# Performance work log

Measured on AMD Instinct MI355X. Metric: run time of the kernel, lower is better.

## Reference

```python
import jax, jax.numpy as jnp
import numpy as np

NUM_HEADS = 4
NUM_GROUPS = 8
EPS = 1e-5


def group_norm(x, w, b):
    # x: [N, C, H, W], normalize over (C//G, H, W) per group
    N, C, H, W = x.shape
    xg = x.reshape(N, NUM_GROUPS, C // NUM_GROUPS, H, W)
    mu = jnp.mean(xg, axis=(2, 3, 4), keepdims=True)
    var = jnp.var(xg, axis=(2, 3, 4), keepdims=True)
    xn = ((xg - mu) * jax.lax.rsqrt(var + EPS)).reshape(N, C, H, W)
    return xn * w[None, :, None, None] + b[None, :, None, None]


def conv1x1(x, w, b):
    # x: [N, C, H, W], w: [Cout, Cin], b: [Cout]
    return jnp.einsum('nchw,dc->ndhw', x, w) + b[None, :, None, None]


def setup_inputs() -> dict:
    key = jax.random.key(0)
    ks = jax.random.split(key, 12)
    N, C, H, W = 2, 256, 64, 64
    s = 1.0 / np.sqrt(C)
    inp = {
        'x': jax.random.normal(ks[0], (N, C, H, W), jnp.float32),
        'mask': jax.random.randint(ks[1], (N, 1, H, W), 0, 2, jnp.int32),
        'norm_w': jnp.ones((C,), jnp.float32),
        'norm_b': jnp.zeros((C,), jnp.float32),
        'q_w': jax.random.normal(ks[2], (C, C), jnp.float32) * s,
        'q_b': jnp.zeros((C,), jnp.float32),
        'k_w': jax.random.normal(ks[3], (C, C), jnp.float32) * s,
        'k_b': jnp.zeros((C,), jnp.float32),
        'v_w': jax.random.normal(ks[4], (C, C), jnp.float32) * s,
        'v_b': jnp.zeros((C,), jnp.float32),
        'p_w': jax.random.normal(ks[5], (C, C), jnp.float32) * s,
        'p_b': jnp.zeros((C,), jnp.float32),
    }
    return inp


def reference(x, mask, norm_w, norm_b, q_w, q_b, k_w, k_b, v_w, v_b, p_w, p_b):
    N, C, H, W = x.shape
    hd = C // NUM_HEADS  # head dim
    L = H * W
    xn = group_norm(x, norm_w, norm_b)
    q = conv1x1(xn, q_w, q_b).reshape(N, NUM_HEADS, hd, L)
    k = conv1x1(xn, k_w, k_b).reshape(N, NUM_HEADS, hd, L)
    v = conv1x1(xn, v_w, v_b).reshape(N, NUM_HEADS, hd, L)
    scores = jnp.einsum('nhcl,nhck->nhlk', q, k) * (hd ** -0.5)
    probs = jax.nn.softmax(scores, axis=-1)
    out = jnp.einsum('nhlk,nhck->nhcl', probs, v).reshape(N, C, H, W)
    out = conv1x1(out, p_w, p_b)
    return (x + out, mask)
```

## Files before the change

kernel.cpp:

```cpp
#include <hip/hip_runtime.h>
#include <hip/hip_bf16.h>

#define NBATCH 2
#define CCH    256
#define LLEN   4096
#define NGROUP 8
#define CPG    32
#define NHEAD  4
#define HD     64
#define GEPS   1e-5f
#define QSCALE 0.18033688011112042f


typedef short bf16x8 __attribute__((ext_vector_type(8)));
typedef float f32x4  __attribute__((ext_vector_type(4)));

__device__ __forceinline__ unsigned short f2b(float f) {
  unsigned u = __float_as_uint(f);
  u += 0x7FFFu + ((u >> 16) & 1u);
  return (unsigned short)(u >> 16);
}
__device__ __forceinline__ unsigned cvtpk(float lo, float hi) {
  unsigned r;
  asm("v_cvt_pk_bf16_f32 %0, %1, %2" : "=v"(r) : "v"(lo), "v"(hi));
  return r;
}
__device__ __forceinline__ float exp2_(float x) {
#if __has_builtin(__builtin_amdgcn_exp2f)
  return __builtin_amdgcn_exp2f(x);
#else
  return exp2f(x);
#endif
}

__global__ __launch_bounds__(256) void setup_kernel(const float* __restrict__ x,
                                                    float* __restrict__ part) {
  __shared__ float rs[4], rss[4];
  const int sb = blockIdx.x;
  const int t = threadIdx.x;
  const int gidx = sb >> 4, sub = sb & 15;
  const float4* xp = (const float4*)(x + (size_t)gidx * (CPG * LLEN)) + (size_t)sub * 2048;
  float s = 0.f, ss = 0.f;
  for (int i = t; i < 2048; i += 256) {
    const float4 v = xp[i];
    s += v.x + v.y + v.z + v.w;
    ss = fmaf(v.x, v.x, ss);
    ss = fmaf(v.y, v.y, ss);
    ss = fmaf(v.z, v.z, ss);
    ss = fmaf(v.w, v.w, ss);
  }
#pragma unroll
  for (int off = 32; off; off >>= 1) {
    s  += __shfl_down(s, off);
    ss += __shfl_down(ss, off);
  }
  if ((t & 63) == 0) { rs[t >> 6] = s; rss[t >> 6] = ss; }
  __syncthreads();
  if (t == 0) {
    part[sb * 2 + 0] = rs[0] + rs[1] + rs[2] + rs[3];
    part[sb * 2 + 1] = rss[0] + rss[1] + rss[2] + rss[3];
  }
}

__global__ __launch_bounds__(256) void gn_apply_kernel(
    const float* __restrict__ x, const float* __restrict__ w,
    const float* __restrict__ b, const float* __restrict__ part,
    const float* __restrict__ qw, const float* __restrict__ kw,
    const float* __restrict__ vw, const float* __restrict__ pw,
    const float* __restrict__ qb, const float* __restrict__ kb,
    const float* __restrict__ vb, const float* __restrict__ pb,
    const int* __restrict__ mask,
    unsigned short* __restrict__ xn16, unsigned short* __restrict__ w16,
    float* __restrict__ bias_ws, float* __restrict__ out2) {
  __shared__ float tile[32][68];
  const int bx = blockIdx.x;
  const int t = threadIdx.x;
  if (bx < 1024) {
    const int lx = bx & 63, cy = (bx >> 6) & 7, n = bx >> 9;
    const int l0 = lx * 64, c0 = cy * 32;
    const int g16 = n * 8 + cy;
    float s = 0.f, ss = 0.f;
#pragma unroll
    for (int i = 0; i < 16; i++) {
      s  += part[(g16 * 16 + i) * 2 + 0];
      ss += part[(g16 * 16 + i) * 2 + 1];
    }
    const float inv_cnt = 1.0f / (float)(CPG * LLEN);
    const float mu = s * inv_cnt;
    const float rsg = rsqrtf(ss * inv_cnt - mu * mu + GEPS);
    const int cl = t >> 3, l8 = t & 7;
    const float aa = rsg * w[c0 + cl];
    const float dd = b[c0 + cl] - mu * aa;
    const float* xrow = x + ((size_t)n * CCH + c0 + cl) * LLEN + l0;
#pragma unroll
    for (int i = 0; i < 2; i++) {
      const int ll = (l8 + 8 * i) * 4;
      float4 v = *(const float4*)(xrow + ll);
      v.x = fmaf(v.x, aa, dd);
      v.y = fmaf(v.y, aa, dd);
      v.z = fmaf(v.z, aa, dd);
      v.w = fmaf(v.w, aa, dd);
      *(float4*)&tile[cl][ll] = v;
    }
    __syncthreads();
    const int l = t & 63, cg = t >> 6;
    const int labs = l0 + l;
    bf16x8 ov;
#pragma unroll
    for (int j = 0; j < 8; j++) ov[j] = (short)f2b(tile[cg * 8 + j][l]);
    const size_t pos = (((size_t)n * 256 + (labs >> 4)) * 8 + (c0 >> 5)) * 512 +
                       ((labs & 15) + 16 * cg) * 8;
    *(bf16x8*)(xn16 + pos) = ov;
  } else if (bx < 1280) {
    const int sb = bx - 1024;
    const int idx = sb * 256 + t;
    const int m = idx >> 14;
    const int rem = idx & 16383;
    const int cout = rem >> 6;
    const int ch4 = (rem & 63) << 2;
    const float* srcp = (m == 0) ? qw : (m == 1) ? kw : (m == 2) ? vw : pw;
    const float sc = (m == 0) ? QSCALE : 1.0f;
    const float4 v = ((const float4*)srcp)[(size_t)cout * 64 + (ch4 >> 2)];
    unsigned short* dst = w16 +
        ((size_t)(m * 16 + (cout >> 4)) * 8 + (ch4 >> 5)) * 512 +
        ((cout & 15) + 16 * ((ch4 >> 3) & 3)) * 8 + (ch4 & 7);
    uint2 wd;
    wd.x = cvtpk(v.x * sc, v.y * sc);
    wd.y = cvtpk(v.z * sc, v.w * sc);
    *(uint2*)dst = wd;
    if (sb == 0) {
      bias_ws[t]       = qb[t] * QSCALE;
      bias_ws[256 + t] = kb[t];
      bias_ws[512 + t] = vb[t];
      bias_ws[768 + t] = pb[t];
    }
  } else {
    const int i = (bx - 1280) * 256 + t;
    out2[i] = (float)mask[i];
  }
}

__global__ __launch_bounds__(256, 4) void qkv_mfma_kernel(
    const unsigned short* __restrict__ xn16,
    const unsigned short* __restrict__ w16,
    const float* __restrict__ bias_ws,
    unsigned short* __restrict__ q16,
    unsigned short* __restrict__ k16,
    unsigned short* __restrict__ v16) {
  const int t = threadIdx.x;
  const int lane = t & 63, wv = t >> 6;
  const int col = lane & 15, quad = lane >> 4;
  const int m0 = blockIdx.x * 32;
  const int wsel = blockIdx.y;
  const int n = m0 >> 12;
  const int m16b = (m0 & 4095) >> 4;
  const int l0 = m0 & 4095;

  const unsigned short* xnb = xn16 + (((size_t)n * 256 + m16b) * 8) * 512 + lane * 8;
  const unsigned short* wb  = w16 + ((size_t)(wsel * 16 + wv * 4) * 8) * 512 + lane * 8;

  f32x4 acc[2][4];
#pragma unroll
  for (int mt = 0; mt < 2; mt++)
#pragma unroll
    for (int ct = 0; ct < 4; ct++) acc[mt][ct] = {0.f, 0.f, 0.f, 0.f};

#pragma unroll
  for (int kc = 0; kc < 8; kc++) {
    bf16x8 xf[2], wf[4];
    xf[0] = *(const bf16x8*)(xnb + (size_t)kc * 512);
    xf[1] = *(const bf16x8*)(xnb + (size_t)(8 + kc) * 512);
#pragma unroll
    for (int ct = 0; ct < 4; ct++)
      wf[ct] = *(const bf16x8*)(wb + (size_t)(ct * 8 + kc) * 512);
#pragma unroll
    for (int mt = 0; mt < 2; mt++)
#pragma unroll
      for (int ct = 0; ct < 4; ct++)
        acc[mt][ct] = (wsel < 2)
            ? __builtin_amdgcn_mfma_f32_16x16x32_bf16(wf[ct], xf[mt], acc[mt][ct], 0, 0, 0)
            : __builtin_amdgcn_mfma_f32_16x16x32_bf16(xf[mt], wf[ct], acc[mt][ct], 0, 0, 0);
  }

  if (wsel < 2) {
    unsigned short* dst = (wsel == 0) ? q16 : k16;
#pragma unroll
    for (int ct = 0; ct < 4; ct++) {
      const float4 b4 = *(const float4*)&bias_ws[wsel * CCH + wv * 64 + ct * 16 + quad * 4];
#pragma unroll
      for (int mt = 0; mt < 2; mt++) {
        uint2 wd;
        wd.x = cvtpk(acc[mt][ct][0] + b4.x, acc[mt][ct][1] + b4.y);
        wd.y = cvtpk(acc[mt][ct][2] + b4.z, acc[mt][ct][3] + b4.w);
        *(uint2*)(dst + ((size_t)(n * 256 + m16b + mt) * 8 + wv * 2 + (ct >> 1)) * 512 +
                  (col + 16 * ((ct & 1) * 2 + (quad >> 1))) * 8 + (quad & 1) * 4) = wd;
      }
    }
  } else {
#pragma unroll
    for (int ct = 0; ct < 4; ct++) {
      const float bv = bias_ws[2 * CCH + wv * 64 + ct * 16 + col];
#pragma unroll
      for (int mt = 0; mt < 2; mt++) {
        uint2 wd;
        wd.x = cvtpk(acc[mt][ct][0] + bv, acc[mt][ct][1] + bv);
        wd.y = cvtpk(acc[mt][ct][2] + bv, acc[mt][ct][3] + bv);
        *(uint2*)(v16 + (((size_t)n * 128 + (l0 >> 5)) * 16 + wv * 4 + ct) * 512 +
                  (col + 16 * (mt * 2 + (quad >> 1))) * 8 + (quad & 1) * 4) = wd;
      }
    }
  }
}

__global__ __launch_bounds__(256, 2) void attn_mfma_kernel(
    const unsigned short* __restrict__ q16,
    const unsigned short* __restrict__ k16,
    const unsigned short* __restrict__ v16,
    unsigned short* __restrict__ o16) {
  __shared__ __align__(16) unsigned char shraw[20480];
  f32x4 (*red)[4][64] = (f32x4 (*)[4][64])shraw;
  f32x4 (*lred)[64] = (f32x4 (*)[64])(shraw + 16384);
  const int t = threadIdx.x;
  const int lane = t & 63, wv = t >> 6;
  const int col = lane & 15, quad = lane >> 4;
  const int fid = blockIdx.y * gridDim.x + blockIdx.x;
  const int nh = fid & 7, qx = fid >> 3;
  const int n = nh >> 2, h = nh & 3;
  const int hc = h * HD;
  const int qt0 = qx * 4;

  const unsigned short* qb = q16 + (size_t)n * (256 * 8 * 512);
  const unsigned short* kb = k16 + (size_t)n * (256 * 8 * 512);
  const unsigned short* vb = v16 + (size_t)n * (128 * 16 * 512);

  bf16x8 bq[4][2];
#pragma unroll
  for (int qt = 0; qt < 4; qt++)
#pragma unroll
    for (int ks = 0; ks < 2; ks++)
      bq[qt][ks] = *(const bf16x8*)(qb + ((size_t)(qt0 + qt) * 8 + h * 2 + ks) * 512 + lane * 8);

  bf16x8 bones;
#pragma unroll
  for (int i = 0; i < 8; i++) bones[i] = (short)0x3F80;
  const f32x4 zf = {0.f, 0.f, 0.f, 0.f};

  f32x4 o[4][4], lacc[4];
#pragma unroll
  for (int qt = 0; qt < 4; qt++) {
    lacc[qt] = {0.f, 0.f, 0.f, 0.f};
#pragma unroll
    for (int ct = 0; ct < 4; ct++) o[qt][ct] = {0.f, 0.f, 0.f, 0.f};
  }

  const unsigned short* kp = kb + ((size_t)(wv * 64) * 8 + h * 2) * 512 + lane * 8;
  const unsigned short* vp = vb + ((size_t)(wv * 32) * 16 + h * 4) * 512 + lane * 8;

  bf16x8 kA[2][2], kB[2][2], vA[4], vB[4];
  auto loadK = [&](bf16x8 (&kr)[2][2], const unsigned short* p) {
#pragma unroll
    for (int kt = 0; kt < 2; kt++)
#pragma unroll
      for (int ks = 0; ks < 2; ks++)
        kr[kt][ks] = *(const bf16x8*)(p + kt * 4096 + ks * 512);
  };
  auto loadV = [&](bf16x8 (&vv)[4], const unsigned short* p) {
#pragma unroll
    for (int ct = 0; ct < 4; ct++) vv[ct] = *(const bf16x8*)(p + ct * 512);
  };

  auto chunk = [&](bf16x8 (&kr)[2][2], bf16x8 (&vv)[4]) {
    bf16x8 pa[4];
#pragma unroll
    for (int qt = 0; qt < 4; qt++) {
      unsigned a0, a1, b0, b1;
      {
        f32x4 s = __builtin_amdgcn_mfma_f32_16x16x32_bf16(kr[0][0], bq[qt][0], zf, 0, 0, 0);
        s = __builtin_amdgcn_mfma_f32_16x16x32_bf16(kr[0][1], bq[qt][1], s, 0, 0, 0);
        a0 = cvtpk(exp2_(s[0]), exp2_(s[1]));
        a1 = cvtpk(exp2_(s[2]), exp2_(s[3]));
      }
      {
        f32x4 s = __builtin_amdgcn_mfma_f32_16x16x32_bf16(kr[1][0], bq[qt][0], zf, 0, 0, 0);
        s = __builtin_amdgcn_mfma_f32_16x16x32_bf16(kr[1][1], bq[qt][1], s, 0, 0, 0);
        b0 = cvtpk(exp2_(s[0]), exp2_(s[1]));
        b1 = cvtpk(exp2_(s[2]), exp2_(s[3]));
      }
      auto r0 = __builtin_amdgcn_permlane32_swap(a0, b0, false, false);
      auto s0 = __builtin_amdgcn_permlane16_swap(r0[0], r0[1], false, false);
      auto r1 = __builtin_amdgcn_permlane32_swap(a1, b1, false, false);
      auto s1 = __builtin_amdgcn_permlane16_swap(r1[0], r1[1], false, false);
      union { unsigned u[4]; bf16x8 v; } pu;
      pu.u[0] = s0[0];
      pu.u[1] = s1[0];
      pu.u[2] = s0[1];
      pu.u[3] = s1[1];
      pa[qt] = pu.v;
    }
    __builtin_amdgcn_s_setprio(1);
#pragma unroll
    for (int qt = 0; qt < 4; qt++) {
      lacc[qt] = __builtin_amdgcn_mfma_f32_16x16x32_bf16(pa[qt], bones, lacc[qt], 0, 0, 0);
#pragma unroll
      for (int ct = 0; ct < 4; ct++)
        o[qt][ct] = __builtin_amdgcn_mfma_f32_16x16x32_bf16(pa[qt], vv[ct], o[qt][ct], 0, 0, 0);
    }
    __builtin_amdgcn_s_setprio(0);
  };

  loadK(kA, kp);
  loadV(vA, vp);
  for (int it = 0; it < 30; it += 2) {
    loadK(kB, kp + 8192);
    loadV(vB, vp + 8192);
    chunk(kA, vA);
    kp += 16384;
    vp += 16384;
    loadK(kA, kp);
    loadV(vA, vp);
    chunk(kB, vB);
  }
  loadK(kB, kp + 8192);
  loadV(vB, vp + 8192);
  chunk(kA, vA);
  chunk(kB, vB);

  const int cch = hc + wv * 16 + col;
  const int lquad16 = 16 * ((cch >> 3) & 3);
  const size_t ctile = cch >> 5;
#pragma unroll
  for (int qt = 0; qt < 4; qt++) {
    __syncthreads();
#pragma unroll
    for (int ct = 0; ct < 4; ct++) red[wv][ct][lane] = o[qt][ct];
    lred[wv][lane] = lacc[qt];
    __syncthreads();
    f32x4 os = red[0][wv][lane];
    os += red[1][wv][lane];
    os += red[2][wv][lane];
    os += red[3][wv][lane];
    f32x4 ls = lred[0][lane];
    ls += lred[1][lane];
    ls += lred[2][lane];
    ls += lred[3][lane];
    const size_t base = (((size_t)n * 256 + qt0 + qt) * 8 + ctile) * 512 + (cch & 7);
#pragma unroll
    for (int r = 0; r < 4; r++)
      o16[base + ((quad * 4 + r) + lquad16) * 8] = f2b(os[r] / ls[r]);
  }
}

__global__ __launch_bounds__(256, 4) void proj_mfma_kernel(
    const unsigned short* __restrict__ o16,
    const unsigned short* __restrict__ w16,
    const float* __restrict__ pbias,
    const float* __restrict__ x,
    float* __restrict__ out) {
  const int t = threadIdx.x;
  const int lane = t & 63, wv = t >> 6;
  const int col = lane & 15, quad = lane >> 4;
  const int m0 = blockIdx.x * 32;
  const int by = blockIdx.y;
  const int co0 = by * 64;
  const int n = m0 >> 12, l0 = m0 & 4095;

  const unsigned short* ob = o16 + (size_t)n * (256 * 8 * 512);
  const unsigned short* wb = w16 + ((size_t)(48 + by * 4 + wv) * 8) * 512 + lane * 8;

  f32x4 acc[2];
#pragma unroll
  for (int i = 0; i < 2; i++) acc[i] = {0.f, 0.f, 0.f, 0.f};

#pragma unroll
  for (int kc = 0; kc < 8; kc++) {
    const bf16x8 aw = *(const bf16x8*)(wb + (size_t)kc * 512);
#pragma unroll
    for (int lt = 0; lt < 2; lt++) {
      const bf16x8 bo = *(const bf16x8*)(ob + ((size_t)((l0 >> 4) + lt) * 8 + kc) * 512 + lane * 8);
      acc[lt] = __builtin_amdgcn_mfma_f32_16x16x32_bf16(aw, bo, acc[lt], 0, 0, 0);
    }
  }
#pragma unroll
  for (int lt = 0; lt < 2; lt++)
#pragma unroll
    for (int r = 0; r < 4; r++) {
      const int cout = co0 + wv * 16 + quad * 4 + r;
      const size_t idx = ((size_t)(n * CCH + cout)) * LLEN + l0 + lt * 16 + col;
      out[idx] = acc[lt][r] + pbias[cout] + x[idx];
    }
}

extern "C" void kernel_launch(void* const* d_in, const int* in_sizes, int n_in,
                              void* d_out, int out_size, void* d_ws, size_t ws_size,
                              hipStream_t stream) {
  (void)in_sizes; (void)n_in; (void)out_size; (void)ws_size;
  const float* x      = (const float*)d_in[0];
  const int*   mask   = (const int*)d_in[1];
  const float* norm_w = (const float*)d_in[2];
  const float* norm_b = (const float*)d_in[3];
  const float* q_w    = (const float*)d_in[4];
  const float* q_b    = (const float*)d_in[5];
  const float* k_w    = (const float*)d_in[6];
  const float* k_b    = (const float*)d_in[7];
  const float* v_w    = (const float*)d_in[8];
  const float* v_b    = (const float*)d_in[9];
  const float* p_w    = (const float*)d_in[10];
  const float* p_b    = (const float*)d_in[11];

  const size_t TSZ = (size_t)NBATCH * LLEN * CCH;
  unsigned short* xn16 = (unsigned short*)d_ws;
  unsigned short* q16  = xn16 + TSZ;
  unsigned short* k16  = q16 + TSZ;
  unsigned short* v16  = k16 + TSZ;
  unsigned short* o16  = v16 + TSZ;
  unsigned short* w16  = o16 + TSZ;
  float* bias_ws = (float*)(w16 + 4 * 65536);
  float* part    = bias_ws + 1024;

  float* out  = (float*)d_out;
  float* out2 = out + TSZ;

  setup_kernel<<<256, 256, 0, stream>>>(x, part);
  gn_apply_kernel<<<1312, 256, 0, stream>>>(
      x, norm_w, norm_b, part, q_w, k_w, v_w, p_w, q_b, k_b, v_b, p_b,
      mask, xn16, w16, bias_ws, out2);
  qkv_mfma_kernel<<<dim3((NBATCH * LLEN) / 32, 3), 256, 0, stream>>>(
      xn16, w16, bias_ws, q16, k16, v16);
  attn_mfma_kernel<<<dim3(LLEN / 64, NBATCH * NHEAD), 256, 0, stream>>>(
      q16, k16, v16, o16);
  proj_mfma_kernel<<<dim3((NBATCH * LLEN) / 32, CCH / 64), 256, 0, stream>>>(
      o16, w16, bias_ws + 768, x, out);
}
```

Measured before the change: 142.5 us.

## Fuse group-norm stats into apply kernel via atomics; software-pipeline attention loop

Merges the separate group-norm statistics kernel into the apply kernel. Each block accumulates partial sums with atomics, then spins on a per-group counter until all 64 blocks of its group have contributed. This saves one launch and a second read of x, but relies on every block being co-resident, since the spin-wait can deadlock otherwise. The attention inner loop is also split into QK-exp, permute and PV stages, software-pipelined across two buffers so exp and permlane work overlaps the PV MFMAs.

```diff
diff --git a/kernel.cpp b/kernel.cpp
--- a/kernel.cpp
+++ b/kernel.cpp
@@ -33,87 +33,51 @@
 #endif
 }
 
-__global__ __launch_bounds__(256) void setup_kernel(const float* __restrict__ x,
-                                                    float* __restrict__ part) {
-  __shared__ float rs[4], rss[4];
-  const int sb = blockIdx.x;
-  const int t = threadIdx.x;
-  const int gidx = sb >> 4, sub = sb & 15;
-  const float4* xp = (const float4*)(x + (size_t)gidx * (CPG * LLEN)) + (size_t)sub * 2048;
-  float s = 0.f, ss = 0.f;
-  for (int i = t; i < 2048; i += 256) {
-    const float4 v = xp[i];
-    s += v.x + v.y + v.z + v.w;
-    ss = fmaf(v.x, v.x, ss);
-    ss = fmaf(v.y, v.y, ss);
-    ss = fmaf(v.z, v.z, ss);
-    ss = fmaf(v.w, v.w, ss);
-  }
-#pragma unroll
-  for (int off = 32; off; off >>= 1) {
-    s  += __shfl_down(s, off);
-    ss += __shfl_down(ss, off);
-  }
-  if ((t & 63) == 0) { rs[t >> 6] = s; rss[t >> 6] = ss; }
-  __syncthreads();
-  if (t == 0) {
-    part[sb * 2 + 0] = rs[0] + rs[1] + rs[2] + rs[3];
-    part[sb * 2 + 1] = rss[0] + rss[1] + rss[2] + rss[3];
-  }
-}
-
-__global__ __launch_bounds__(256) void gn_apply_kernel(
-    const float* __restrict__ x, const float* __restrict__ w,
-    const float* __restrict__ b, const float* __restrict__ part,
+__global__ __launch_bounds__(256, 8) void gn_fused_kernel(
+    const float* __restrict__ x, const float* __restrict__ gw,
+    const float* __restrict__ gb,
     const float* __restrict__ qw, const float* __restrict__ kw,
     const float* __restrict__ vw, const float* __restrict__ pw,
     const float* __restrict__ qb, const float* __restrict__ kb,
     const float* __restrict__ vb, const float* __restrict__ pb,
     const int* __restrict__ mask,
     unsigned short* __restrict__ xn16, unsigned short* __restrict__ w16,
-    float* __restrict__ bias_ws, float* __restrict__ out2) {
+    float* __restrict__ bias_ws, float* __restrict__ gstat,
+    unsigned* __restrict__ gcnt, float* __restrict__ out2) {
   __shared__ float tile[32][68];
-  const int bx = blockIdx.x;
-  const int t = threadIdx.x;
-  if (bx < 1024) {
-    const int lx = bx & 63, cy = (bx >> 6) & 7, n = bx >> 9;
-    const int l0 = lx * 64, c0 = cy * 32;
-    const int g16 = n * 8 + cy;
-    float s = 0.f, ss = 0.f;
-#pragma unroll
-    for (int i = 0; i < 16; i++) {
-      s  += part[(g16 * 16 + i) * 2 + 0];
-      ss += part[(g16 * 16 + i) * 2 + 1];
-    }
-    const float inv_cnt = 1.0f / (float)(CPG * LLEN);
-    const float mu = s * inv_cnt;
-    const float rsg = rsqrtf(ss * inv_cnt - mu * mu + GEPS);
-    const int cl = t >> 3, l8 = t & 7;
-    const float aa = rsg * w[c0 + cl];
-    const float dd = b[c0 + cl] - mu * aa;
-    const float* xrow = x + ((size_t)n * CCH + c0 + cl) * LLEN + l0;
-#pragma unroll
-    for (int i = 0; i < 2; i++) {
-      const int ll = (l8 + 8 * i) * 4;
-      float4 v = *(const float4*)(xrow + ll);
-      v.x = fmaf(v.x, aa, dd);
-      v.y = fmaf(v.y, aa, dd);
-      v.z = fmaf(v.z, aa, dd);
-      v.w = fmaf(v.w, aa, dd);
-      *(float4*)&tile[cl][ll] = v;
-    }
-    __syncthreads();
-    const int l = t & 63, cg = t >> 6;
-    const int labs = l0 + l;
-    bf16x8 ov;
-#pragma unroll
-    for (int j = 0; j < 8; j++) ov[j] = (short)f2b(tile[cg * 8 + j][l]);
-    const size_t pos = (((size_t)n * 256 + (labs >> 4)) * 8 + (c0 >> 5)) * 512 +
-                       ((labs & 15) + 16 * cg) * 8;
-    *(bf16x8*)(xn16 + pos) = ov;
-  } else if (bx < 1280) {
-    const int sb = bx - 1024;
-    const int idx = sb * 256 + t;
+  __shared__ float sred[8];
+  __shared__ float smu, srsg;
+  const int bx = blockIdx.x, t = threadIdx.x;
+  const int lx = bx & 63, cy = (bx >> 6) & 7, n = bx >> 9;
+  const int l0 = lx * 64, c0 = cy * 32;
+  const int g = n * 8 + cy;
+  const int cl = t >> 3, l8 = t & 7;
+  const float* xrow = x + ((size_t)n * CCH + c0 + cl) * LLEN + l0;
+  const float4 va = ((const float4*)xrow)[l8];
+  const float4 vb2 = ((const float4*)xrow)[l8 + 8];
+  float s = va.x + va.y + va.z + va.w + vb2.x + vb2.y + vb2.z + vb2.w;
+  float ss = 0.f;
+  ss = fmaf(va.x, va.x, ss);  ss = fmaf(va.y, va.y, ss);
+  ss = fmaf(va.z, va.z, ss);  ss = fmaf(va.w, va.w, ss);
+  ss = fmaf(vb2.x, vb2.x, ss); ss = fmaf(vb2.y, vb2.y, ss);
+  ss = fmaf(vb2.z, vb2.z, ss); ss = fmaf(vb2.w, vb2.w, ss);
+#pragma unroll
+  for (int off = 32; off; off >>= 1) {
+    s  += __shfl_down(s, off);
+    ss += __shfl_down(ss, off);
+  }
+  if ((t & 63) == 0) { sred[t >> 6] = s; sred[4 + (t >> 6)] = ss; }
+  __syncthreads();
+  if (t == 0) {
+    const float S = sred[0] + sred[1] + sred[2] + sred[3];
+    const float SS = sred[4] + sred[5] + sred[6] + sred[7];
+    atomicAdd(&gstat[g], S);
+    atomicAdd(&gstat[16 + g], SS);
+    __threadfence();
+    __hip_atomic_fetch_add(&gcnt[g], 1u, __ATOMIC_RELEASE, __HIP_MEMORY_SCOPE_AGENT);
+  }
+  if (t < 64) {
+    const int idx = bx * 64 + t;
     const int m = idx >> 14;
     const int rem = idx & 16383;
     const int cout = rem >> 6;
@@ -128,16 +92,50 @@
     wd.x = cvtpk(v.x * sc, v.y * sc);
     wd.y = cvtpk(v.z * sc, v.w * sc);
     *(uint2*)dst = wd;
-    if (sb == 0) {
-      bias_ws[t]       = qb[t] * QSCALE;
-      bias_ws[256 + t] = kb[t];
-      bias_ws[512 + t] = vb[t];
-      bias_ws[768 + t] = pb[t];
-    }
-  } else {
-    const int i = (bx - 1280) * 256 + t;
+  } else if (t < 72) {
+    const int i = bx * 8 + (t - 64);
     out2[i] = (float)mask[i];
-  }
+  } else if (t == 72) {
+    const int m = bx >> 8, c = bx & 255;
+    bias_ws[bx] = (m == 0) ? qb[c] * QSCALE : (m == 1) ? kb[c]
+                : (m == 2) ? vb[c] : pb[c];
+  }
+  const float wc = gw[c0 + cl], bc = gb[c0 + cl];
+  if (t == 0) {
+    while (__hip_atomic_load(&gcnt[g], __ATOMIC_ACQUIRE,
+                             __HIP_MEMORY_SCOPE_AGENT) < 64u)
+      __builtin_amdgcn_s_sleep(2);
+    const float S = __hip_atomic_load(&gstat[g], __ATOMIC_RELAXED,
+                                      __HIP_MEMORY_SCOPE_AGENT);
+    const float SS = __hip_atomic_load(&gstat[16 + g], __ATOMIC_RELAXED,
+                                       __HIP_MEMORY_SCOPE_AGENT);
+    const float inv = 1.0f / (float)(CPG * LLEN);
+    const float mu = S * inv;
+    smu = mu;
+    srsg = rsqrtf(SS * inv - mu * mu + GEPS);
+  }
+  __syncthreads();
+  const float aa = srsg * wc;
+  const float dd = bc - smu * aa;
+  {
+    float4 u = va, v = vb2;
+    u.x = fmaf(u.x, aa, dd); u.y = fmaf(u.y, aa, dd);
+    u.z = fmaf(u.z, aa, dd); u.w = fmaf(u.w, aa, dd);
+    v.x = fmaf(v.x, aa, dd); v.y = fmaf(v.y, aa, dd);
+    v.z = fmaf(v.z, aa, dd); v.w = fmaf(v.w, aa, dd);
+    *(float4*)&tile[cl][l8 * 4] = u;
+    *(float4*)&tile[cl][(l8 + 8) * 4] = v;
+  }
+  __syncthreads();
+  const int l = t & 63, cg = t >> 6;
+  const int labs = l0 + l;
+  union { unsigned u[4]; bf16x8 v; } ov;
+#pragma unroll
+  for (int j = 0; j < 4; j++)
+    ov.u[j] = cvtpk(tile[cg * 8 + 2 * j][l], tile[cg * 8 + 2 * j + 1][l]);
+  const size_t pos = (((size_t)n * 256 + (labs >> 4)) * 8 + (c0 >> 5)) * 512 +
+                     ((labs & 15) + 16 * cg) * 8;
+  *(bf16x8*)(xn16 + pos) = ov.v;
 }
 
 __global__ __launch_bounds__(256, 4) void qkv_mfma_kernel(
@@ -257,6 +255,9 @@
   const unsigned short* vp = vb + ((size_t)(wv * 32) * 16 + h * 4) * 512 + lane * 8;
 
   bf16x8 kA[2][2], kB[2][2], vA[4], vB[4];
+  unsigned pkA[4][4], pkB[4][4];
+  bf16x8 paA[4], paB[4];
+
   auto loadK = [&](bf16x8 (&kr)[2][2], const unsigned short* p) {
 #pragma unroll
     for (int kt = 0; kt < 2; kt++)
@@ -268,27 +269,25 @@
 #pragma unroll
     for (int ct = 0; ct < 4; ct++) vv[ct] = *(const bf16x8*)(p + ct * 512);
   };
-
-  auto chunk = [&](bf16x8 (&kr)[2][2], bf16x8 (&vv)[4]) {
-    bf16x8 pa[4];
+  auto QKE = [&](unsigned (&pk)[4][4], bf16x8 (&kr)[2][2]) {
 #pragma unroll
     for (int qt = 0; qt < 4; qt++) {
-      unsigned a0, a1, b0, b1;
-      {
-        f32x4 s = __builtin_amdgcn_mfma_f32_16x16x32_bf16(kr[0][0], bq[qt][0], zf, 0, 0, 0);
-        s = __builtin_amdgcn_mfma_f32_16x16x32_bf16(kr[0][1], bq[qt][1], s, 0, 0, 0);
-        a0 = cvtpk(exp2_(s[0]), exp2_(s[1]));
-        a1 = cvtpk(exp2_(s[2]), exp2_(s[3]));
-      }
-      {
-        f32x4 s = __builtin_amdgcn_mfma_f32_16x16x32_bf16(kr[1][0], bq[qt][0], zf, 0, 0, 0);
-        s = __builtin_amdgcn_mfma_f32_16x16x32_bf16(kr[1][1], bq[qt][1], s, 0, 0, 0);
-        b0 = cvtpk(exp2_(s[0]), exp2_(s[1]));
-        b1 = cvtpk(exp2_(s[2]), exp2_(s[3]));
-      }
-      auto r0 = __builtin_amdgcn_permlane32_swap(a0, b0, false, false);
+      f32x4 sa = __builtin_amdgcn_mfma_f32_16x16x32_bf16(kr[0][0], bq[qt][0], zf, 0, 0, 0);
+      sa = __builtin_amdgcn_mfma_f32_16x16x32_bf16(kr[0][1], bq[qt][1], sa, 0, 0, 0);
+      f32x4 sb = __builtin_amdgcn_mfma_f32_16x16x32_bf16(kr[1][0], bq[qt][0], zf, 0, 0, 0);
+      sb = __builtin_amdgcn_mfma_f32_16x16x32_bf16(kr[1][1], bq[qt][1], sb, 0, 0, 0);
+      pk[qt][0] = cvtpk(exp2_(sa[0]), exp2_(sa[1]));
+      pk[qt][1] = cvtpk(exp2_(sa[2]), exp2_(sa[3]));
+      pk[qt][2] = cvtpk(exp2_(sb[0]), exp2_(sb[1]));
+      pk[qt][3] = cvtpk(exp2_(sb[2]), exp2_(sb[3]));
+    }
+  };
+  auto PERM = [&](bf16x8 (&pa)[4], unsigned (&pk)[4][4]) {
+#pragma unroll
+    for (int qt = 0; qt < 4; qt++) {
+      auto r0 = __builtin_amdgcn_permlane32_swap(pk[qt][0], pk[qt][2], false, false);
       auto s0 = __builtin_amdgcn_permlane16_swap(r0[0], r0[1], false, false);
-      auto r1 = __builtin_amdgcn_permlane32_swap(a1, b1, false, false);
+      auto r1 = __builtin_amdgcn_permlane32_swap(pk[qt][1], pk[qt][3], false, false);
       auto s1 = __builtin_amdgcn_permlane16_swap(r1[0], r1[1], false, false);
       union { unsigned u[4]; bf16x8 v; } pu;
       pu.u[0] = s0[0];
@@ -297,6 +296,8 @@
       pu.u[3] = s1[1];
       pa[qt] = pu.v;
     }
+  };
+  auto PV = [&](bf16x8 (&pa)[4], bf16x8 (&vv)[4]) {
     __builtin_amdgcn_s_setprio(1);
 #pragma unroll
     for (int qt = 0; qt < 4; qt++) {
@@ -308,22 +309,27 @@
     __builtin_amdgcn_s_setprio(0);
   };
 
-  loadK(kA, kp);
-  loadV(vA, vp);
+  loadK(kA, kp); loadV(vA, vp);
+  QKE(pkA, kA);
+  loadK(kB, kp + 8192); loadV(vB, vp + 8192);
   for (int it = 0; it < 30; it += 2) {
-    loadK(kB, kp + 8192);
-    loadV(vB, vp + 8192);
-    chunk(kA, vA);
-    kp += 16384;
-    vp += 16384;
-    loadK(kA, kp);
-    loadV(vA, vp);
-    chunk(kB, vB);
-  }
-  loadK(kB, kp + 8192);
-  loadV(vB, vp + 8192);
-  chunk(kA, vA);
-  chunk(kB, vB);
+    PERM(paA, pkA);
+    loadK(kA, kp + 16384);
+    QKE(pkB, kB);
+    PV(paA, vA);
+    loadK(kB, kp + 24576);
+    loadV(vA, vp + 16384);
+    PERM(paB, pkB);
+    QKE(pkA, kA);
+    PV(paB, vB);
+    loadV(vB, vp + 24576);
+    kp += 16384; vp += 16384;
+  }
+  PERM(paA, pkA);
+  QKE(pkB, kB);
+  PV(paA, vA);
+  PERM(paB, pkB);
+  PV(paB, vB);
 
   const int cch = hc + wv * 16 + col;
   const int lquad16 = 16 * ((cch >> 3) & 3);
@@ -415,15 +421,16 @@
   unsigned short* o16  = v16 + TSZ;
   unsigned short* w16  = o16 + TSZ;
   float* bias_ws = (float*)(w16 + 4 * 65536);
-  float* part    = bias_ws + 1024;
+  float* gstat   = bias_ws + 1024;
+  unsigned* gcnt = (unsigned*)(gstat + 32);
 
   float* out  = (float*)d_out;
   float* out2 = out + TSZ;
 
-  setup_kernel<<<256, 256, 0, stream>>>(x, part);
-  gn_apply_kernel<<<1312, 256, 0, stream>>>(
-      x, norm_w, norm_b, part, q_w, k_w, v_w, p_w, q_b, k_b, v_b, p_b,
-      mask, xn16, w16, bias_ws, out2);
+  hipMemsetAsync(gstat, 0, (32 + 16) * sizeof(float), stream);
+  gn_fused_kernel<<<1024, 256, 0, stream>>>(
+      x, norm_w, norm_b, q_w, k_w, v_w, p_w, q_b, k_b, v_b, p_b,
+      mask, xn16, w16, bias_ws, gstat, gcnt, out2);
   qkv_mfma_kernel<<<dim3((NBATCH * LLEN) / 32, 3), 256, 0, stream>>>(
       xn16, w16, bias_ws, q16, k16, v16);
   attn_mfma_kernel<<<dim3(LLEN / 64, NBATCH * NHEAD), 256, 0, stream>>>(
```

Result: slower. 192.6 us (+35.1%).

## Software-pipeline attention loop so QK^T/exp of next chunk overlaps PV of current

Applied to the files above, without the earlier changes.

Splits the per-chunk attention body into QK+exp, permute, and PV stages, then reorders the main loop so the score/exp computation for chunk i+1 is issued alongside the PV MFMAs of chunk i. The goal is to overlap the transcendental and VALU work with matrix-core work and to hide the dependency stall between the score MFMAs and their exp. It keeps more registers live (two packed-probability buffers and two permuted operand sets), which risks lower occupancy or spills.

```diff
diff --git a/kernel.cpp b/kernel.cpp
--- a/kernel.cpp
+++ b/kernel.cpp
@@ -257,6 +257,9 @@
   const unsigned short* vp = vb + ((size_t)(wv * 32) * 16 + h * 4) * 512 + lane * 8;
 
   bf16x8 kA[2][2], kB[2][2], vA[4], vB[4];
+  unsigned pkA[4][4], pkB[4][4];
+  bf16x8 paA[4], paB[4];
+
   auto loadK = [&](bf16x8 (&kr)[2][2], const unsigned short* p) {
 #pragma unroll
     for (int kt = 0; kt < 2; kt++)
@@ -268,27 +271,25 @@
 #pragma unroll
     for (int ct = 0; ct < 4; ct++) vv[ct] = *(const bf16x8*)(p + ct * 512);
   };
-
-  auto chunk = [&](bf16x8 (&kr)[2][2], bf16x8 (&vv)[4]) {
-    bf16x8 pa[4];
+  auto QKE = [&](unsigned (&pk)[4][4], bf16x8 (&kr)[2][2]) {
 #pragma unroll
     for (int qt = 0; qt < 4; qt++) {
-      unsigned a0, a1, b0, b1;
-      {
-        f32x4 s = __builtin_amdgcn_mfma_f32_16x16x32_bf16(kr[0][0], bq[qt][0], zf, 0, 0, 0);
-        s = __builtin_amdgcn_mfma_f32_16x16x32_bf16(kr[0][1], bq[qt][1], s, 0, 0, 0);
-        a0 = cvtpk(exp2_(s[0]), exp2_(s[1]));
-        a1 = cvtpk(exp2_(s[2]), exp2_(s[3]));
-      }
-      {
-        f32x4 s = __builtin_amdgcn_mfma_f32_16x16x32_bf16(kr[1][0], bq[qt][0], zf, 0, 0, 0);
-        s = __builtin_amdgcn_mfma_f32_16x16x32_bf16(kr[1][1], bq[qt][1], s, 0, 0, 0);
-        b0 = cvtpk(exp2_(s[0]), exp2_(s[1]));
-        b1 = cvtpk(exp2_(s[2]), exp2_(s[3]));
-      }
-      auto r0 = __builtin_amdgcn_permlane32_swap(a0, b0, false, false);
+      f32x4 sa = __builtin_amdgcn_mfma_f32_16x16x32_bf16(kr[0][0], bq[qt][0], zf, 0, 0, 0);
+      sa = __builtin_amdgcn_mfma_f32_16x16x32_bf16(kr[0][1], bq[qt][1], sa, 0, 0, 0);
+      f32x4 sb = __builtin_amdgcn_mfma_f32_16x16x32_bf16(kr[1][0], bq[qt][0], zf, 0, 0, 0);
+      sb = __builtin_amdgcn_mfma_f32_16x16x32_bf16(kr[1][1], bq[qt][1], sb, 0, 0, 0);
+      pk[qt][0] = cvtpk(exp2_(sa[0]), exp2_(sa[1]));
+      pk[qt][1] = cvtpk(exp2_(sa[2]), exp2_(sa[3]));
+      pk[qt][2] = cvtpk(exp2_(sb[0]), exp2_(sb[1]));
+      pk[qt][3] = cvtpk(exp2_(sb[2]), exp2_(sb[3]));
+    }
+  };
+  auto PERM = [&](bf16x8 (&pa)[4], unsigned (&pk)[4][4]) {
+#pragma unroll
+    for (int qt = 0; qt < 4; qt++) {
+      auto r0 = __builtin_amdgcn_permlane32_swap(pk[qt][0], pk[qt][2], false, false);
       auto s0 = __builtin_amdgcn_permlane16_swap(r0[0], r0[1], false, false);
-      auto r1 = __builtin_amdgcn_permlane32_swap(a1, b1, false, false);
+      auto r1 = __builtin_amdgcn_permlane32_swap(pk[qt][1], pk[qt][3], false, false);
       auto s1 = __builtin_amdgcn_permlane16_swap(r1[0], r1[1], false, false);
       union { unsigned u[4]; bf16x8 v; } pu;
       pu.u[0] = s0[0];
@@ -297,6 +298,8 @@
       pu.u[3] = s1[1];
       pa[qt] = pu.v;
     }
+  };
+  auto PV = [&](bf16x8 (&pa)[4], bf16x8 (&vv)[4]) {
     __builtin_amdgcn_s_setprio(1);
 #pragma unroll
     for (int qt = 0; qt < 4; qt++) {
@@ -308,22 +311,27 @@
     __builtin_amdgcn_s_setprio(0);
   };
 
-  loadK(kA, kp);
-  loadV(vA, vp);
+  loadK(kA, kp); loadV(vA, vp);
+  QKE(pkA, kA);
+  loadK(kB, kp + 8192); loadV(vB, vp + 8192);
   for (int it = 0; it < 30; it += 2) {
-    loadK(kB, kp + 8192);
-    loadV(vB, vp + 8192);
-    chunk(kA, vA);
-    kp += 16384;
-    vp += 16384;
-    loadK(kA, kp);
-    loadV(vA, vp);
-    chunk(kB, vB);
-  }
-  loadK(kB, kp + 8192);
-  loadV(vB, vp + 8192);
-  chunk(kA, vA);
-  chunk(kB, vB);
+    PERM(paA, pkA);
+    loadK(kA, kp + 16384);
+    QKE(pkB, kB);
+    PV(paA, vA);
+    loadK(kB, kp + 24576);
+    loadV(vA, vp + 16384);
+    PERM(paB, pkB);
+    QKE(pkA, kA);
+    PV(paB, vB);
+    loadV(vB, vp + 24576);
+    kp += 16384; vp += 16384;
+  }
+  PERM(paA, pkA);
+  QKE(pkB, kB);
+  PV(paA, vA);
+  PERM(paB, pkB);
+  PV(paB, vB);
 
   const int cch = hc + wv * 16 + col;
   const int lquad16 = 16 * ((cch >> 3) & 3);
```

New measurement: 143.7 us. No clear change (+0.8%).

## Fuse Q projection into attention kernel prologue, drop Q global buffer

Applied to the files above, without the earlier changes.

Q is no longer computed by the QKV kernel and written to global memory. Each attention block now computes its 64-query, single-head Q tile from the normalized input and Q weights with MFMA, rearranges it with permlane swaps into the expected fragment layout, and stages it through shared memory. This removes a third of the QKV grid plus the Q write and read traffic. In exchange, each attention block adds a short GEMM prologue and a barrier before its main loop.

```diff
diff --git a/kernel.cpp b/kernel.cpp
--- a/kernel.cpp
+++ b/kernel.cpp
@@ -144,14 +144,13 @@
     const unsigned short* __restrict__ xn16,
     const unsigned short* __restrict__ w16,
     const float* __restrict__ bias_ws,
-    unsigned short* __restrict__ q16,
     unsigned short* __restrict__ k16,
     unsigned short* __restrict__ v16) {
   const int t = threadIdx.x;
   const int lane = t & 63, wv = t >> 6;
   const int col = lane & 15, quad = lane >> 4;
   const int m0 = blockIdx.x * 32;
-  const int wsel = blockIdx.y;
+  const int wsel = blockIdx.y + 1;
   const int n = m0 >> 12;
   const int m16b = (m0 & 4095) >> 4;
   const int l0 = m0 & 4095;
@@ -177,13 +176,12 @@
     for (int mt = 0; mt < 2; mt++)
 #pragma unroll
       for (int ct = 0; ct < 4; ct++)
-        acc[mt][ct] = (wsel < 2)
+        acc[mt][ct] = (wsel == 1)
             ? __builtin_amdgcn_mfma_f32_16x16x32_bf16(wf[ct], xf[mt], acc[mt][ct], 0, 0, 0)
             : __builtin_amdgcn_mfma_f32_16x16x32_bf16(xf[mt], wf[ct], acc[mt][ct], 0, 0, 0);
   }
 
-  if (wsel < 2) {
-    unsigned short* dst = (wsel == 0) ? q16 : k16;
+  if (wsel == 1) {
 #pragma unroll
     for (int ct = 0; ct < 4; ct++) {
       const float4 b4 = *(const float4*)&bias_ws[wsel * CCH + wv * 64 + ct * 16 + quad * 4];
@@ -192,7 +190,7 @@
         uint2 wd;
         wd.x = cvtpk(acc[mt][ct][0] + b4.x, acc[mt][ct][1] + b4.y);
         wd.y = cvtpk(acc[mt][ct][2] + b4.z, acc[mt][ct][3] + b4.w);
-        *(uint2*)(dst + ((size_t)(n * 256 + m16b + mt) * 8 + wv * 2 + (ct >> 1)) * 512 +
+        *(uint2*)(k16 + ((size_t)(n * 256 + m16b + mt) * 8 + wv * 2 + (ct >> 1)) * 512 +
                   (col + 16 * ((ct & 1) * 2 + (quad >> 1))) * 8 + (quad & 1) * 4) = wd;
       }
     }
@@ -213,13 +211,16 @@
 }
 
 __global__ __launch_bounds__(256, 2) void attn_mfma_kernel(
-    const unsigned short* __restrict__ q16,
+    const unsigned short* __restrict__ xn16,
+    const unsigned short* __restrict__ w16,
+    const float* __restrict__ bias_ws,
     const unsigned short* __restrict__ k16,
     const unsigned short* __restrict__ v16,
     unsigned short* __restrict__ o16) {
   __shared__ __align__(16) unsigned char shraw[20480];
   f32x4 (*red)[4][64] = (f32x4 (*)[4][64])shraw;
   f32x4 (*lred)[64] = (f32x4 (*)[64])(shraw + 16384);
+  bf16x8 (*qlds)[2][64] = (bf16x8 (*)[2][64])shraw;
   const int t = threadIdx.x;
   const int lane = t & 63, wv = t >> 6;
   const int col = lane & 15, quad = lane >> 4;
@@ -229,21 +230,55 @@
   const int hc = h * HD;
   const int qt0 = qx * 4;
 
-  const unsigned short* qb = q16 + (size_t)n * (256 * 8 * 512);
+  const unsigned short* xb = xn16 + (size_t)n * (256 * 8 * 512);
   const unsigned short* kb = k16 + (size_t)n * (256 * 8 * 512);
   const unsigned short* vb = v16 + (size_t)n * (128 * 16 * 512);
 
-  bf16x8 bq[4][2];
-#pragma unroll
-  for (int qt = 0; qt < 4; qt++)
-#pragma unroll
-    for (int ks = 0; ks < 2; ks++)
-      bq[qt][ks] = *(const bf16x8*)(qb + ((size_t)(qt0 + qt) * 8 + h * 2 + ks) * 512 + lane * 8);
-
   bf16x8 bones;
 #pragma unroll
   for (int i = 0; i < 8; i++) bones[i] = (short)0x3F80;
   const f32x4 zf = {0.f, 0.f, 0.f, 0.f};
+
+  {
+    const unsigned short* xq = xb + ((size_t)(qt0 + wv) * 8) * 512 + lane * 8;
+    bf16x8 xf[8];
+#pragma unroll
+    for (int kc = 0; kc < 8; kc++) xf[kc] = *(const bf16x8*)(xq + (size_t)kc * 512);
+#pragma unroll
+    for (int ks = 0; ks < 2; ks++) {
+      const int g = h * 2 + ks;
+      f32x4 da = zf, db = zf;
+#pragma unroll
+      for (int kc = 0; kc < 8; kc++) {
+        const bf16x8 wf0 = *(const bf16x8*)(w16 + ((size_t)((2 * g + 0) * 8 + kc)) * 512 + lane * 8);
+        const bf16x8 wf1 = *(const bf16x8*)(w16 + ((size_t)((2 * g + 1) * 8 + kc)) * 512 + lane * 8);
+        da = __builtin_amdgcn_mfma_f32_16x16x32_bf16(wf0, xf[kc], da, 0, 0, 0);
+        db = __builtin_amdgcn_mfma_f32_16x16x32_bf16(wf1, xf[kc], db, 0, 0, 0);
+      }
+      const float4 ba = *(const float4*)&bias_ws[g * 32 + 0 * 16 + quad * 4];
+      const float4 bb = *(const float4*)&bias_ws[g * 32 + 1 * 16 + quad * 4];
+      const unsigned a0 = cvtpk(da[0] + ba.x, da[1] + ba.y);
+      const unsigned a1 = cvtpk(da[2] + ba.z, da[3] + ba.w);
+      const unsigned b0 = cvtpk(db[0] + bb.x, db[1] + bb.y);
+      const unsigned b1 = cvtpk(db[2] + bb.z, db[3] + bb.w);
+      auto r0 = __builtin_amdgcn_permlane32_swap(a0, b0, false, false);
+      auto s0 = __builtin_amdgcn_permlane16_swap(r0[0], r0[1], false, false);
+      auto r1 = __builtin_amdgcn_permlane32_swap(a1, b1, false, false);
+      auto s1 = __builtin_amdgcn_permlane16_swap(r1[0], r1[1], false, false);
+      union { unsigned u[4]; bf16x8 v; } pu;
+      pu.u[0] = s0[0];
+      pu.u[1] = s1[0];
+      pu.u[2] = s0[1];
+      pu.u[3] = s1[1];
+      qlds[wv][ks][lane] = pu.v;
+    }
+  }
+  __syncthreads();
+  bf16x8 bq[4][2];
+#pragma unroll
+  for (int qt = 0; qt < 4; qt++)
+#pragma unroll
+    for (int ks = 0; ks < 2; ks++) bq[qt][ks] = qlds[qt][ks][lane];
 
   f32x4 o[4][4], lacc[4];
 #pragma unroll
@@ -409,8 +444,7 @@
 
   const size_t TSZ = (size_t)NBATCH * LLEN * CCH;
   unsigned short* xn16 = (unsigned short*)d_ws;
-  unsigned short* q16  = xn16 + TSZ;
-  unsigned short* k16  = q16 + TSZ;
+  unsigned short* k16  = xn16 + TSZ;
   unsigned short* v16  = k16 + TSZ;
   unsigned short* o16  = v16 + TSZ;
   unsigned short* w16  = o16 + TSZ;
@@ -424,10 +458,10 @@
   gn_apply_kernel<<<1312, 256, 0, stream>>>(
       x, norm_w, norm_b, part, q_w, k_w, v_w, p_w, q_b, k_b, v_b, p_b,
       mask, xn16, w16, bias_ws, out2);
-  qkv_mfma_kernel<<<dim3((NBATCH * LLEN) / 32, 3), 256, 0, stream>>>(
-      xn16, w16, bias_ws, q16, k16, v16);
+  qkv_mfma_kernel<<<dim3((NBATCH * LLEN) / 32, 2), 256, 0, stream>>>(
+      xn16, w16, bias_ws, k16, v16);
   attn_mfma_kernel<<<dim3(LLEN / 64, NBATCH * NHEAD), 256, 0, stream>>>(
-      q16, k16, v16, o16);
+      xn16, w16, bias_ws, k16, v16, o16);
   proj_mfma_kernel<<<dim3((NBATCH * LLEN) / 32, CCH / 64), 256, 0, stream>>>(
       o16, w16, bias_ws + 768, x, out);
 }
```

After: 143.7 us. Within noise of the previous version (+0.8%).
